# Kernel tuning notes

Measured on AMD Instinct MI355X. Metric: run time of the kernel, lower is better.

Reference implementation:

```python
import jax, jax.numpy as jnp
import numpy as np

N = 4096      # num_nodes
U = 64        # num_units
IN = 2        # input_dim
DIM = U + IN  # 66
H = 4         # attention heads
ALPHA = 0.2   # leaky slope inside attention scores
SLOPE = 0.01  # nn.LeakyReLU() default for subnet activations
NEG_INF = -9e15


def setup_inputs() -> dict:
    key = jax.random.key(0)
    ks = jax.random.split(key, 20)
    def gn(k, shape, fan):
        return jax.random.normal(k, shape, dtype=jnp.float32) / np.float32(np.sqrt(fan))
    adj = jax.random.randint(ks[2], (N, N), 0, 2, dtype=jnp.int32)
    adj = jnp.maximum(adj, jnp.eye(N, dtype=jnp.int32))  # ensure self-loops
    return {
        "inputs": jax.random.normal(ks[0], (1, N * IN), dtype=jnp.float32),
        "hx": jax.random.normal(ks[1], (1, N, U), dtype=jnp.float32),
        "adj": adj,
        "m1_W": gn(ks[3], (H, DIM, DIM), DIM),
        "m1_a1": gn(ks[4], (H, DIM), DIM),
        "m1_a2": gn(ks[5], (H, DIM), DIM),
        "m1_Wout": gn(ks[6], (H * DIM, DIM), H * DIM),
        "m1_ao1": gn(ks[7], (DIM,), DIM),
        "m1_ao2": gn(ks[8], (DIM,), DIM),
        "m2_W": gn(ks[9], (H, DIM, DIM), DIM),
        "m2_a1": gn(ks[10], (H, DIM), DIM),
        "m2_a2": gn(ks[11], (H, DIM), DIM),
        "m2_Wout": gn(ks[12], (H * DIM, DIM), H * DIM),
        "m2_ao1": gn(ks[13], (DIM,), DIM),
        "m2_ao2": gn(ks[14], (DIM,), DIM),
        "g1_W": gn(ks[15], (DIM, 2 * U), DIM),
        "g1_b": jnp.zeros((2 * U,), dtype=jnp.float32),
        "g2_W": gn(ks[16], (DIM, U), DIM),
        "g2_b": jnp.zeros((U,), dtype=jnp.float32),
    }


def gat_layer(x, W, a1, a2, mask):
    # x: [N,Fin], W: [Fin,Fout], a1/a2: [Fout], mask: [N,N] bool
    h = x @ W                                   # [N,Fout]
    f1 = h @ a1                                 # [N] source term
    f2 = h @ a2                                 # [N] target term
    e = jax.nn.leaky_relu(f1[:, None] + f2[None, :], ALPHA)  # [N,N]
    e = jnp.where(mask, e, NEG_INF)
    attn = jax.nn.softmax(e, axis=-1)
    return attn @ h                             # [N,Fout]


def subnet(x, W, a1, a2, Wout, ao1, ao2, mask):
    # multi-head GAT, concat heads, activation, output GAT layer, activation
    heads = jax.vmap(gat_layer, in_axes=(None, 0, 0, 0, None))(x, W, a1, a2, mask)  # [H,N,DIM]
    hcat = jnp.transpose(heads, (1, 0, 2)).reshape(x.shape[0], -1)                   # [N,H*DIM]
    hcat = jax.nn.leaky_relu(hcat, SLOPE)
    out = gat_layer(hcat, Wout, ao1, ao2, mask)                                      # [N,DIM]
    return jax.nn.leaky_relu(out, SLOPE)


def reference(inputs, hx, adj, m1_W, m1_a1, m1_a2, m1_Wout, m1_ao1, m1_ao2,
              m2_W, m2_a1, m2_a2, m2_Wout, m2_ao1, m2_ao2,
              g1_W, g1_b, g2_W, g2_b):
    mask = adj > 0
    xi = inputs.reshape(N, IN)
    xh = hx.reshape(N, U)
    # _GAT1: concat(inputs, hx) -> GATSubNet1 -> linear -> sigmoid -> split r,u
    x1 = jnp.concatenate([xi, xh], axis=-1)                 # [N,DIM]
    g1 = subnet(x1, m1_W, m1_a1, m1_a2, m1_Wout, m1_ao1, m1_ao2, mask)
    value = jax.nn.sigmoid(g1 @ g1_W + g1_b)                # [N,2U]
    r, u = value[:, :U], value[:, U:]
    # _GAT2: concat(inputs, r*hx) -> GATSubNet2 -> linear -> tanh
    x2 = jnp.concatenate([xi, r * xh], axis=-1)             # [N,DIM]
    g2 = subnet(x2, m2_W, m2_a1, m2_a2, m2_Wout, m2_ao1, m2_ao2, mask)
    c = jnp.tanh(g2 @ g2_W + g2_b)                          # [N,U]
    new_state = u * xh + (1.0 - u) * c
    return new_state.reshape(1, N, U)
```

## Files before the change

### kernel.cpp

```cpp
#include <hip/hip_runtime.h>
#include <hip/hip_bf16.h>

constexpr int kN = 4096;
constexpr int kDim = 66;
constexpr int kH = 4;
constexpr int kU = 64;
constexpr float kAlpha = 0.2f;
constexpr float kSlope = 0.01f;
constexpr float kLog2e = 1.44269504f;

typedef _Float16 half8 __attribute__((ext_vector_type(8)));
typedef _Float16 half2t __attribute__((ext_vector_type(2)));
typedef __attribute__((ext_vector_type(4))) float floatx4;

__device__ inline unsigned int fkey(float f){
  unsigned int u = __float_as_uint(f);
  return (u & 0x80000000u) ? ~u : (u | 0x80000000u);
}
__device__ inline float funkey(unsigned int k){
  unsigned int u = (k & 0x80000000u) ? (k ^ 0x80000000u) : ~k;
  return __uint_as_float(u);
}

__global__ void setup_k(const int* __restrict__ adj, unsigned long long* __restrict__ packed,
                        const float* __restrict__ in2, const float* __restrict__ hx,
                        _Float16* __restrict__ x1b, _Float16* __restrict__ x2b,
                        const float* __restrict__ m1W, const float* __restrict__ m1a1, const float* __restrict__ m1a2,
                        const float* __restrict__ m1Wo, const float* __restrict__ m1ao1, const float* __restrict__ m1ao2,
                        const float* __restrict__ m2W, const float* __restrict__ m2a1, const float* __restrict__ m2a2,
                        const float* __restrict__ m2Wo, const float* __restrict__ m2ao1, const float* __restrict__ m2ao2,
                        const float* __restrict__ g1W, const float* __restrict__ g1b,
                        const float* __restrict__ g2W, const float* __restrict__ g2b,
                        _Float16* __restrict__ B1t, _Float16* __restrict__ B1t2,
                        _Float16* __restrict__ B2t, _Float16* __restrict__ B2t2,
                        _Float16* __restrict__ Bgt, _Float16* __restrict__ Bft,
                        unsigned int* __restrict__ fmaxbuf){
  int bb = blockIdx.x, t = threadIdx.x;
  if (bb < 16384){
    int gid = bb * 256 + t;
    unsigned long long m = __ballot(adj[gid] != 0);
    if ((t & 63) == 0) packed[gid >> 6] = m;
    return;
  }
  if (bb < 16384 + 1024){
    int i = (bb - 16384) * 4 + (t >> 6);
    int c = t & 63;
    x1b[(size_t)i * 96 + 2 + c] = (_Float16)hx[(size_t)i * kU + c];
    if (c < 2){
      _Float16 xv = (_Float16)in2[i * 2 + c];
      x1b[(size_t)i * 96 + c] = xv;
      x2b[(size_t)i * 96 + c] = xv;
    }
    if (c < 30){
      x1b[(size_t)i * 96 + 66 + c] = (_Float16)0.f;
      x2b[(size_t)i * 96 + 66 + c] = (_Float16)0.f;
    }
    return;
  }
  int b = bb - (16384 + 1024);
  if (b < 8){
    int m = b & 3;
    const float* W  = (b < 4 ? m1W  : m2W)  + (size_t)m * kDim * kDim;
    const float* a1 = (b < 4 ? m1a1 : m2a1) + m * kDim;
    const float* a2 = (b < 4 ? m1a2 : m2a2) + m * kDim;
    _Float16* Bo = (b < 4 ? B1t : B1t2) + (size_t)m * 80 * 96;
    __shared__ float Ws[kDim * kDim];
    __shared__ float wa1s[kDim], wa2s[kDim];
    for (int z = t; z < kDim * kDim; z += 256) Ws[z] = W[z];
    __syncthreads();
    if (t < kDim){
      float s1 = 0.f, s2 = 0.f;
      for (int d = 0; d < kDim; d++){ float wv = Ws[t * kDim + d]; s1 += wv * a1[d]; s2 += wv * a2[d]; }
      wa1s[t] = s1; wa2s[t] = s2;
    }
    __syncthreads();
    for (int z = t; z < 80 * 96; z += 256){
      int nn = z / 96, k = z % 96;
      float val = 0.f;
      if (k < kDim){
        if (nn < kDim) val = Ws[k * kDim + nn];
        else if (nn == 66) val = wa1s[k];
        else if (nn == 67) val = wa2s[k];
      }
      Bo[z] = (_Float16)val;
    }
  } else if (b < 10){
    const float* Wo  = (b == 8 ? m1Wo  : m2Wo);
    const float* ao1 = (b == 8 ? m1ao1 : m2ao1);
    const float* ao2 = (b == 8 ? m1ao2 : m2ao2);
    _Float16* Bo = (b == 8 ? B2t : B2t2);
    __shared__ float wo1s[264], wo2s[264];
    for (int k = t; k < 264; k += 256){
      float s1 = 0.f, s2 = 0.f;
      for (int d = 0; d < kDim; d++){ float wv = Wo[(size_t)k * kDim + d]; s1 += wv * ao1[d]; s2 += wv * ao2[d]; }
      wo1s[k] = s1; wo2s[k] = s2;
    }
    __syncthreads();
    for (int z = t; z < 80 * 288; z += 256){
      int nn = z / 288, k = z % 288;
      float val = 0.f;
      if (k < 264){
        if (nn < kDim) val = Wo[(size_t)k * kDim + nn];
        else if (nn == 66) val = wo1s[k];
        else if (nn == 67) val = wo2s[k];
      }
      Bo[z] = (_Float16)val;
    }
  } else if (b == 10){
    for (int z = t; z < 128 * 96; z += 256){
      int nn = z / 96, k = z % 96;
      float val = 0.f;
      if (k < kDim) val = g1W[k * 128 + nn];
      else if (k == 66) val = g1b[nn];
      Bgt[z] = (_Float16)val;
    }
  } else {
    if (t < 16) fmaxbuf[t] = 0u;
    for (int z = t; z < 64 * 96; z += 256){
      int nn = z / 96, k = z % 96;
      float val = 0.f;
      if (k < kDim) val = g2W[k * 64 + nn];
      else if (k == 66) val = g2b[nn];
      Bft[z] = (_Float16)val;
    }
  }
}

template<int KSTEPS, int NT, int EPI>
__global__ __launch_bounds__(256) void gemm_k(
    const _Float16* __restrict__ A, const _Float16* __restrict__ Bt,
    void* __restrict__ p0, void* __restrict__ p1, void* __restrict__ p2,
    const float* __restrict__ aux, unsigned int* __restrict__ fmaxp)
{
  constexpr int KP = KSTEPS * 32;
  const int m = blockIdx.y;
  const int i0 = blockIdx.x * 64;
  const int t = threadIdx.x;
  const int w = t >> 6, lane = t & 63, q = lane >> 4, n = lane & 15;
  const int arow = i0 + w * 16 + n;
  const _Float16* Ar = A + (size_t)arow * KP;
  const _Float16* Bm = Bt + (size_t)m * (NT * 16) * KP;
  floatx4 acc[NT];
  #pragma unroll
  for (int v = 0; v < NT; v++) acc[v] = (floatx4){0.f, 0.f, 0.f, 0.f};
  #pragma unroll
  for (int ks = 0; ks < KSTEPS; ks++){
    half8 af = *(const half8*)&Ar[ks * 32 + q * 8];
    #pragma unroll
    for (int nt = 0; nt < NT; nt++){
      half8 bf = *(const half8*)&Bm[(size_t)(nt * 16 + n) * KP + ks * 32 + q * 8];
      acc[nt] = __builtin_amdgcn_mfma_f32_16x16x32_f16(af, bf, acc[nt], 0, 0, 0);
    }
  }
  const int ib = i0 + w * 16 + q * 4;
  if constexpr (EPI == 0){
    _Float16* Ht = (_Float16*)p0 + (size_t)m * 68 * kN;
    float* f1 = (float*)p1 + (size_t)m * kN;
    float* f2 = (float*)p2 + (size_t)m * kN;
    float lm = -3e38f;
    #pragma unroll
    for (int nt = 0; nt < NT; nt++){
      int c = nt * 16 + n;
      if (c < kDim){
        union { _Float16 h[4]; uint2 v; } pk;
        pk.h[0] = (_Float16)acc[nt][0]; pk.h[1] = (_Float16)acc[nt][1];
        pk.h[2] = (_Float16)acc[nt][2]; pk.h[3] = (_Float16)acc[nt][3];
        *(uint2*)&Ht[(size_t)c * kN + ib] = pk.v;
      } else if (c == 66){
        float4 fv; fv.x = acc[nt][0] * kLog2e; fv.y = acc[nt][1] * kLog2e;
        fv.z = acc[nt][2] * kLog2e; fv.w = acc[nt][3] * kLog2e;
        *(float4*)&f1[ib] = fv;
        *(uint2*)&Ht[(size_t)66 * kN + ib] = make_uint2(0x3C003C00u, 0x3C003C00u);
      } else if (c == 67){
        float4 fv; fv.x = acc[nt][0] * kLog2e; fv.y = acc[nt][1] * kLog2e;
        fv.z = acc[nt][2] * kLog2e; fv.w = acc[nt][3] * kLog2e;
        *(float4*)&f2[ib] = fv;
        lm = fmaxf(fmaxf(fv.x, fv.y), fmaxf(fv.z, fv.w));
        *(uint2*)&Ht[(size_t)67 * kN + ib] = make_uint2(0u, 0u);
      }
    }
    lm = fmaxf(lm, __shfl_xor(lm, 16));
    lm = fmaxf(lm, __shfl_xor(lm, 32));
    if (lane == 3) atomicMax(&fmaxp[m], fkey(lm));
  } else if constexpr (EPI == 1){
    float* u = (float*)p0;
    _Float16* x2b = (_Float16*)p1;
    #pragma unroll
    for (int nt = 0; nt < NT; nt++){
      int c = nt * 16 + n;
      #pragma unroll
      for (int r = 0; r < 4; r++){
        float v = 1.f / (1.f + __expf(-acc[nt][r]));
        if (c < 64) x2b[(size_t)(ib + r) * 96 + 2 + c] = (_Float16)(v * aux[(size_t)(ib + r) * kU + c]);
        else        u[(size_t)(ib + r) * kU + (c - 64)] = v;
      }
    }
  } else {
    float* outp = (float*)p0;
    const float* u = (const float*)p1;
    #pragma unroll
    for (int nt = 0; nt < NT; nt++){
      int c = nt * 16 + n;
      #pragma unroll
      for (int r = 0; r < 4; r++){
        float cc = tanhf(acc[nt][r]);
        float uv = u[(size_t)(ib + r) * kU + c];
        outp[(size_t)(ib + r) * kU + c] = uv * aux[(size_t)(ib + r) * kU + c] + (1.f - uv) * cc;
      }
    }
  }
}

template<int JSPLIT>
__global__ __launch_bounds__(256, 4) void attn_mfma_k(
    const _Float16* __restrict__ Ht, const float* __restrict__ f1,
    const float* __restrict__ f2, const unsigned int* __restrict__ fmaxu,
    const unsigned long long* __restrict__ packed,
    _Float16* __restrict__ paccb)
{
  constexpr int JR = kN / JSPLIT;
  constexpr int NCH = JR / 128;
  const int m = blockIdx.y, js = blockIdx.z;
  const int i0 = blockIdx.x * 64;
  const int t = threadIdx.x;
  const int w = t >> 6, lane = t & 63, q = lane >> 4, n = lane & 15;
  const int i = i0 + w * 16 + n;
  const _Float16* Hg = Ht + (size_t)m * 68 * kN;
  const float* f2m = f2 + (size_t)m * kN;
  const float f1v = f1[(size_t)m * kN + i];
  const float fmx = funkey(fmaxu[m]);
  const float t0 = f1v + fmx;
  const float S = fmaxf(t0, kAlpha * t0);
  const float A1f = __builtin_amdgcn_exp2f(t0 - S);
  const float A2f = __builtin_amdgcn_exp2f(kAlpha * t0 - S);
  const half2t a1p = { (_Float16)A1f, (_Float16)A1f };
  const half2t a2p = { (_Float16)A2f, (_Float16)A2f };

  __shared__ __align__(16) _Float16 HtL[80 * 136];
  __shared__ __align__(16) _Float16 B1h[128], B2h[128];

  for (int z = t; z < 12 * 136; z += 256) HtL[68 * 136 + z] = (_Float16)0.f;

  floatx4 acc[5];
  #pragma unroll
  for (int v = 0; v < 5; v++) acc[v] = (floatx4){0.f, 0.f, 0.f, 0.f};

  const int jbase = js * JR;
  const unsigned long long* prow = packed + (size_t)i * 64;
  for (int ch = 0; ch < NCH; ch++){
    const int j0 = jbase + ch * 128;
    __syncthreads();
    for (int z = t; z < 68 * 16; z += 256){
      int row = z >> 4, c16 = z & 15;
      *(uint4*)&HtL[row * 136 + c16 * 8] = *(const uint4*)&Hg[(size_t)row * kN + j0 + c16 * 8];
    }
    if (t < 128){
      float v = f2m[j0 + t] - fmx;
      B1h[t] = (_Float16)__builtin_amdgcn_exp2f(v);
      B2h[t] = (_Float16)__builtin_amdgcn_exp2f(kAlpha * v);
    }
    __syncthreads();
    unsigned long long w0 = prow[(j0 >> 6)];
    unsigned long long w1 = prow[(j0 >> 6) + 1];
    #pragma unroll
    for (int ks = 0; ks < 4; ks++){
      unsigned long long wsel = (ks < 2) ? w0 : w1;
      unsigned int bits = (unsigned int)((wsel >> ((ks & 1) * 32 + q * 8)) & 0xffull);
      union { uint4 v; unsigned int u[4]; } b1v, b2v;
      b1v.v = *(const uint4*)&B1h[ks * 32 + q * 8];
      b2v.v = *(const uint4*)&B2h[ks * 32 + q * 8];
      union { half8 s; unsigned int u[4]; } af;
      #pragma unroll
      for (int e = 0; e < 4; e++){
        half2t x1 = __builtin_bit_cast(half2t, b1v.u[e]);
        half2t x2 = __builtin_bit_cast(half2t, b2v.u[e]);
        half2t m1 = x1 * a1p;
        half2t m2 = x2 * a2p;
        half2t pm = __builtin_elementwise_max(m1, m2);
        unsigned int mm = (((bits >> (2 * e)) & 1u) ? 0x0000FFFFu : 0u)
                        | (((bits >> (2 * e + 1)) & 1u) ? 0xFFFF0000u : 0u);
        af.u[e] = __builtin_bit_cast(unsigned int, pm) & mm;
      }
      #pragma unroll
      for (int nt = 0; nt < 5; nt++){
        const half8 bf = *(const half8*)&HtL[(nt * 16 + n) * 136 + ks * 32 + q * 8];
        acc[nt] = __builtin_amdgcn_mfma_f32_16x16x32_f16(af.s, bf, acc[nt], 0, 0, 0);
      }
    }
  }
  _Float16* pw = paccb + ((size_t)(m * JSPLIT + js) * kN + (i0 + w * 16)) * 80;
  #pragma unroll
  for (int nt = 0; nt < 5; nt++){
    if (nt < 4 || n < 4){
      #pragma unroll
      for (int r = 0; r < 4; r++)
        pw[(q * 4 + r) * 80 + nt * 16 + n] = (_Float16)acc[nt][r];
    }
  }
}

template<int JSPLIT>
__global__ void combine_k(const _Float16* __restrict__ paccb, _Float16* __restrict__ outb,
                          int ostride, int ones_col){
  int m = blockIdx.y;
  int i = blockIdx.x * 64 + (threadIdx.x >> 2);
  int cg = threadIdx.x & 3;
  const _Float16* ps[JSPLIT];
  #pragma unroll
  for (int s = 0; s < JSPLIT; s++)
    ps[s] = paccb + ((size_t)(m * JSPLIT + s) * kN + i) * 80;
  float l = 0.f;
  #pragma unroll
  for (int s = 0; s < JSPLIT; s++) l += (float)ps[s][66];
  float inv = 1.f / l;
  _Float16* orow = outb + (size_t)i * ostride + m * kDim;
  #pragma unroll
  for (int cc = 0; cc < 17; cc++){
    int c = cg * 17 + cc;
    if (c < kDim){
      float v = 0.f;
      #pragma unroll
      for (int s = 0; s < JSPLIT; s++) v += (float)ps[s][c];
      v *= inv;
      v = fmaxf(v, kSlope * v);
      orow[c] = (_Float16)v;
    }
  }
  if (ones_col && cg == 3) orow[66] = (_Float16)1.f;
}

extern "C" void kernel_launch(void* const* d_in, const int* in_sizes, int n_in,
                              void* d_out, int out_size, void* d_ws, size_t ws_size,
                              hipStream_t stream){
  const float* inputs  = (const float*)d_in[0];
  const float* hx      = (const float*)d_in[1];
  const int*   adj     = (const int*)d_in[2];
  const float* m1_W    = (const float*)d_in[3];
  const float* m1_a1   = (const float*)d_in[4];
  const float* m1_a2   = (const float*)d_in[5];
  const float* m1_Wout = (const float*)d_in[6];
  const float* m1_ao1  = (const float*)d_in[7];
  const float* m1_ao2  = (const float*)d_in[8];
  const float* m2_W    = (const float*)d_in[9];
  const float* m2_a1   = (const float*)d_in[10];
  const float* m2_a2   = (const float*)d_in[11];
  const float* m2_Wout = (const float*)d_in[12];
  const float* m2_ao1  = (const float*)d_in[13];
  const float* m2_ao2  = (const float*)d_in[14];
  const float* g1_W    = (const float*)d_in[15];
  const float* g1_b    = (const float*)d_in[16];
  const float* g2_W    = (const float*)d_in[17];
  const float* g2_b    = (const float*)d_in[18];
  float* out = (float*)d_out;

  char* ws = (char*)d_ws;
  size_t off = 0;
  auto alloc = [&](size_t bytes) -> void* {
    void* p = ws + off;
    off = (off + bytes + 255) & ~(size_t)255;
    return p;
  };
  unsigned long long* packed = (unsigned long long*)alloc((size_t)kN * 64 * 8);
  _Float16* x1b  = (_Float16*)alloc((size_t)kN * 96 * 2);
  _Float16* x2b  = (_Float16*)alloc((size_t)kN * 96 * 2);
  _Float16* Ht   = (_Float16*)alloc((size_t)kH * 68 * kN * 2);
  _Float16* Hto  = (_Float16*)alloc((size_t)68 * kN * 2);
  _Float16* hcatb= (_Float16*)alloc((size_t)kN * 288 * 2);
  _Float16* gb   = (_Float16*)alloc((size_t)kN * 96 * 2);
  _Float16* g2bv = (_Float16*)alloc((size_t)kN * 96 * 2);
  float* f1   = (float*)alloc((size_t)kH * kN * 4);
  float* f2   = (float*)alloc((size_t)kH * kN * 4);
  float* fo1  = (float*)alloc((size_t)kN * 4);
  float* fo2  = (float*)alloc((size_t)kN * 4);
  unsigned int* fmaxbuf = (unsigned int*)alloc(64);
  float* u    = (float*)alloc((size_t)kN * kU * 4);
  _Float16* paccb = (_Float16*)alloc((size_t)16 * kN * 80 * 2);
  _Float16* B1t  = (_Float16*)alloc((size_t)kH * 80 * 96 * 2);
  _Float16* B1t2 = (_Float16*)alloc((size_t)kH * 80 * 96 * 2);
  _Float16* B2t  = (_Float16*)alloc((size_t)80 * 288 * 2);
  _Float16* B2t2 = (_Float16*)alloc((size_t)80 * 288 * 2);
  _Float16* Bgt  = (_Float16*)alloc((size_t)128 * 96 * 2);
  _Float16* Bft  = (_Float16*)alloc((size_t)64 * 96 * 2);
  (void)ws_size; (void)in_sizes; (void)n_in; (void)out_size;

  setup_k<<<16384 + 1024 + 12, 256, 0, stream>>>(adj, packed, inputs, hx, x1b, x2b,
      m1_W, m1_a1, m1_a2, m1_Wout, m1_ao1, m1_ao2,
      m2_W, m2_a1, m2_a2, m2_Wout, m2_ao1, m2_ao2,
      g1_W, g1_b, g2_W, g2_b,
      B1t, B1t2, B2t, B2t2, Bgt, Bft, fmaxbuf);

  gemm_k<3, 5, 0><<<dim3(64, kH), 256, 0, stream>>>(x1b, B1t, Ht, f1, f2, nullptr, fmaxbuf + 0);
  attn_mfma_k<4><<<dim3(64, kH, 4), 256, 0, stream>>>(Ht, f1, f2, fmaxbuf + 0, packed, paccb);
  combine_k<4><<<dim3(64, kH), 256, 0, stream>>>(paccb, hcatb, 288, 0);
  gemm_k<9, 5, 0><<<dim3(64, 1), 256, 0, stream>>>(hcatb, B2t, Hto, fo1, fo2, nullptr, fmaxbuf + 4);
  attn_mfma_k<8><<<dim3(64, 1, 8), 256, 0, stream>>>(Hto, fo1, fo2, fmaxbuf + 4, packed, paccb);
  combine_k<8><<<dim3(64, 1), 256, 0, stream>>>(paccb, gb, 96, 1);
  gemm_k<3, 8, 1><<<dim3(64, 1), 256, 0, stream>>>(gb, Bgt, u, x2b, nullptr, hx, nullptr);

  gemm_k<3, 5, 0><<<dim3(64, kH), 256, 0, stream>>>(x2b, B1t2, Ht, f1, f2, nullptr, fmaxbuf + 5);
  attn_mfma_k<4><<<dim3(64, kH, 4), 256, 0, stream>>>(Ht, f1, f2, fmaxbuf + 5, packed, paccb);
  combine_k<4><<<dim3(64, kH), 256, 0, stream>>>(paccb, hcatb, 288, 0);
  gemm_k<9, 5, 0><<<dim3(64, 1), 256, 0, stream>>>(hcatb, B2t2, Hto, fo1, fo2, nullptr, fmaxbuf + 9);
  attn_mfma_k<8><<<dim3(64, 1, 8), 256, 0, stream>>>(Hto, fo1, fo2, fmaxbuf + 9, packed, paccb);
  combine_k<8><<<dim3(64, 1), 256, 0, stream>>>(paccb, g2bv, 96, 1);
  gemm_k<3, 4, 2><<<dim3(64, 1), 256, 0, stream>>>(g2bv, Bft, out, u, nullptr, hx, nullptr);
}
```

Baseline: 319.6 us.

## Double-buffer attention tiles via direct global-to-LDS loads with swizzle; vectorize combine

The attention kernel now stages each 128-column chunk of H into LDS with global_load_lds and a double buffer, prefetching the next chunk and its exp terms while MFMAs run on the current one. The LDS layout drops padding in favour of an XOR swizzle, and a shared zero row stands in for the padded rows. The combine kernel reads and writes 16-byte vectors and pads each head to 72 columns, so the concatenated hidden layout and the Wout weight packing are remapped to match. This overlaps the global loads that were previously serialized between barriers, at the cost of a more intricate layout that must stay consistent across kernels.

```diff
diff --git a/kernel.cpp b/kernel.cpp
--- a/kernel.cpp
+++ b/kernel.cpp
@@ -20,6 +20,11 @@
 __device__ inline float funkey(unsigned int k){
   unsigned int u = (k & 0x80000000u) ? (k ^ 0x80000000u) : ~k;
   return __uint_as_float(u);
+}
+
+__device__ __forceinline__ void gld_lds16(const void* g, void* l){
+  __builtin_amdgcn_global_load_lds((const __attribute__((address_space(1))) unsigned int*)g,
+                                   (__attribute__((address_space(3))) unsigned int*)l, 16, 0, 0);
 }
 
 __global__ void setup_k(const int* __restrict__ adj, unsigned long long* __restrict__ packed,
@@ -98,11 +103,13 @@
     __syncthreads();
     for (int z = t; z < 80 * 288; z += 256){
       int nn = z / 288, k = z % 288;
+      int h = k / 72, c = k - h * 72;
       float val = 0.f;
-      if (k < 264){
-        if (nn < kDim) val = Wo[(size_t)k * kDim + nn];
-        else if (nn == 66) val = wo1s[k];
-        else if (nn == 67) val = wo2s[k];
+      if (c < 66){
+        int kk = h * 66 + c;
+        if (nn < kDim) val = Wo[(size_t)kk * kDim + nn];
+        else if (nn == 66) val = wo1s[kk];
+        else if (nn == 67) val = wo2s[kk];
       }
       Bo[z] = (_Float16)val;
     }
@@ -236,58 +243,104 @@
   const half2t a1p = { (_Float16)A1f, (_Float16)A1f };
   const half2t a2p = { (_Float16)A2f, (_Float16)A2f };
 
-  __shared__ __align__(16) _Float16 HtL[80 * 136];
-  __shared__ __align__(16) _Float16 B1h[128], B2h[128];
-
-  for (int z = t; z < 12 * 136; z += 256) HtL[68 * 136 + z] = (_Float16)0.f;
-
-  floatx4 acc[5];
-  #pragma unroll
-  for (int v = 0; v < 5; v++) acc[v] = (floatx4){0.f, 0.f, 0.f, 0.f};
+  __shared__ __align__(16) _Float16 buf[2][68 * 128];
+  __shared__ __align__(16) _Float16 Zro[128];
+  __shared__ __align__(16) _Float16 B1h[2][128], B2h[2][128];
+
+  for (int z = t; z < 128; z += 256) Zro[z] = (_Float16)0.f;
+
+  const int r4 = q;
+  const int cse = n ^ r4;
+  const int cso = cse ^ 4;
 
   const int jbase = js * JR;
   const unsigned long long* prow = packed + (size_t)i * 64;
-  for (int ch = 0; ch < NCH; ch++){
-    const int j0 = jbase + ch * 128;
-    __syncthreads();
-    for (int z = t; z < 68 * 16; z += 256){
-      int row = z >> 4, c16 = z & 15;
-      *(uint4*)&HtL[row * 136 + c16 * 8] = *(const uint4*)&Hg[(size_t)row * kN + j0 + c16 * 8];
-    }
-    if (t < 128){
-      float v = f2m[j0 + t] - fmx;
-      B1h[t] = (_Float16)__builtin_amdgcn_exp2f(v);
-      B2h[t] = (_Float16)__builtin_amdgcn_exp2f(kAlpha * v);
-    }
-    __syncthreads();
-    unsigned long long w0 = prow[(j0 >> 6)];
-    unsigned long long w1 = prow[(j0 >> 6) + 1];
-    #pragma unroll
-    for (int ks = 0; ks < 4; ks++){
-      unsigned long long wsel = (ks < 2) ? w0 : w1;
-      unsigned int bits = (unsigned int)((wsel >> ((ks & 1) * 32 + q * 8)) & 0xffull);
-      union { uint4 v; unsigned int u[4]; } b1v, b2v;
-      b1v.v = *(const uint4*)&B1h[ks * 32 + q * 8];
-      b2v.v = *(const uint4*)&B2h[ks * 32 + q * 8];
-      union { half8 s; unsigned int u[4]; } af;
-      #pragma unroll
-      for (int e = 0; e < 4; e++){
-        half2t x1 = __builtin_bit_cast(half2t, b1v.u[e]);
-        half2t x2 = __builtin_bit_cast(half2t, b2v.u[e]);
-        half2t m1 = x1 * a1p;
-        half2t m2 = x2 * a2p;
-        half2t pm = __builtin_elementwise_max(m1, m2);
-        unsigned int mm = (((bits >> (2 * e)) & 1u) ? 0x0000FFFFu : 0u)
-                        | (((bits >> (2 * e + 1)) & 1u) ? 0xFFFF0000u : 0u);
-        af.u[e] = __builtin_bit_cast(unsigned int, pm) & mm;
-      }
-      #pragma unroll
-      for (int nt = 0; nt < 5; nt++){
-        const half8 bf = *(const half8*)&HtL[(nt * 16 + n) * 136 + ks * 32 + q * 8];
-        acc[nt] = __builtin_amdgcn_mfma_f32_16x16x32_f16(af.s, bf, acc[nt], 0, 0, 0);
-      }
-    }
-  }
+  const int jj = (w << 5) | (lane & 31);
+  const bool blane = (lane & 32) == 0;
+
+#define STAGE_G(PD, CH) do { \
+    const _Float16* gB_ = Hg + jbase + (CH) * 128; \
+    _Pragma("unroll") \
+    for (int kk_ = 0; kk_ < 5; kk_++){ \
+      const int k_ = w + kk_ * 4; \
+      if (k_ < 17){ \
+        const int row_ = k_ * 4 + r4; \
+        const int csw_ = (k_ & 1) ? cso : cse; \
+        gld_lds16(gB_ + (size_t)row_ * kN + csw_ * 8, &buf[(PD)][k_ * 512]); \
+      } \
+    } \
+  } while (0)
+
+  floatx4 acc[5];
+  #pragma unroll
+  for (int v = 0; v < 5; v++) acc[v] = (floatx4){0.f, 0.f, 0.f, 0.f};
+
+  if (blane){
+    const float v_ = f2m[jbase + jj] - fmx;
+    B1h[0][jj] = (_Float16)__builtin_amdgcn_exp2f(v_);
+    B2h[0][jj] = (_Float16)__builtin_amdgcn_exp2f(kAlpha * v_);
+  }
+  STAGE_G(0, 0);
+  __syncthreads();
+
+  int ch = 0;
+#define BODY(P) do { \
+    const int j0_ = jbase + ch * 128; \
+     \
+    float f2v_ = 0.f; \
+    const bool doB_ = (ch + 1 < NCH) && blane; \
+    if (doB_) f2v_ = f2m[j0_ + 128 + jj]; \
+    const unsigned long long w0_ = prow[j0_ >> 6]; \
+    const unsigned long long w1_ = prow[(j0_ >> 6) + 1]; \
+    __builtin_amdgcn_sched_barrier(0); \
+    if (ch + 1 < NCH) STAGE_G((P) ^ 1, ch + 1); \
+    __builtin_amdgcn_sched_barrier(0); \
+    if (doB_){ \
+      const float v_ = f2v_ - fmx; \
+      B1h[(P) ^ 1][jj] = (_Float16)__builtin_amdgcn_exp2f(v_); \
+      B2h[(P) ^ 1][jj] = (_Float16)__builtin_amdgcn_exp2f(kAlpha * v_); \
+    } \
+    const _Float16* bz_ = (n < 4) ? &buf[(P)][(64 + n) * 128] : Zro; \
+    _Pragma("unroll") \
+    for (int ks = 0; ks < 4; ks++){ \
+      const unsigned long long wsel = (ks < 2) ? w0_ : w1_; \
+      const unsigned int bits = (unsigned int)((wsel >> ((ks & 1) * 32 + q * 8)) & 0xffull); \
+      union { uint4 v; unsigned int u[4]; } b1v, b2v; \
+      b1v.v = *(const uint4*)&B1h[(P)][ks * 32 + q * 8]; \
+      b2v.v = *(const uint4*)&B2h[(P)][ks * 32 + q * 8]; \
+      union { half8 s; unsigned int u[4]; } af; \
+      _Pragma("unroll") \
+      for (int e = 0; e < 4; e++){ \
+        half2t x1 = __builtin_bit_cast(half2t, b1v.u[e]); \
+        half2t x2 = __builtin_bit_cast(half2t, b2v.u[e]); \
+        half2t m1 = x1 * a1p; \
+        half2t m2 = x2 * a2p; \
+        half2t pm = __builtin_elementwise_max(m1, m2); \
+        unsigned int mm = (((bits >> (2 * e)) & 1u) ? 0x0000FFFFu : 0u) \
+                        | (((bits >> (2 * e + 1)) & 1u) ? 0xFFFF0000u : 0u); \
+        af.u[e] = __builtin_bit_cast(unsigned int, pm) & mm; \
+      } \
+      const int cs_ = ((ks * 4 + q) ^ (n & 7)) * 8; \
+      _Pragma("unroll") \
+      for (int nt = 0; nt < 4; nt++){ \
+        const half8 bf = *(const half8*)&buf[(P)][(nt * 16 + n) * 128 + cs_]; \
+        acc[nt] = __builtin_amdgcn_mfma_f32_16x16x32_f16(af.s, bf, acc[nt], 0, 0, 0); \
+      } \
+      { const half8 bf4 = *(const half8*)&bz_[cs_]; \
+        acc[4] = __builtin_amdgcn_mfma_f32_16x16x32_f16(af.s, bf4, acc[4], 0, 0, 0); } \
+    } \
+    ch++; \
+    if (ch < NCH) __syncthreads(); \
+  } while (0)
+
+  #pragma unroll 1
+  for (int it = 0; it < NCH / 2; it++){
+    BODY(0);
+    BODY(1);
+  }
+#undef BODY
+#undef STAGE_G
+
   _Float16* pw = paccb + ((size_t)(m * JSPLIT + js) * kN + (i0 + w * 16)) * 80;
   #pragma unroll
   for (int nt = 0; nt < 5; nt++){
@@ -301,32 +354,55 @@
 
 template<int JSPLIT>
 __global__ void combine_k(const _Float16* __restrict__ paccb, _Float16* __restrict__ outb,
-                          int ostride, int ones_col){
-  int m = blockIdx.y;
-  int i = blockIdx.x * 64 + (threadIdx.x >> 2);
-  int cg = threadIdx.x & 3;
-  const _Float16* ps[JSPLIT];
-  #pragma unroll
-  for (int s = 0; s < JSPLIT; s++)
-    ps[s] = paccb + ((size_t)(m * JSPLIT + s) * kN + i) * 80;
-  float l = 0.f;
-  #pragma unroll
-  for (int s = 0; s < JSPLIT; s++) l += (float)ps[s][66];
-  float inv = 1.f / l;
-  _Float16* orow = outb + (size_t)i * ostride + m * kDim;
-  #pragma unroll
-  for (int cc = 0; cc < 17; cc++){
-    int c = cg * 17 + cc;
-    if (c < kDim){
-      float v = 0.f;
+                          int ostride, int headoff, int ones_col){
+  const int m = blockIdx.y;
+  const int t = threadIdx.x;
+  const int ri = t >> 2, cg = t & 3;
+  const int lane = t & 63;
+  const int i = blockIdx.x * 64 + ri;
+  const _Float16* pb = paccb + ((size_t)m * JSPLIT * kN + i) * 80;
+  float accv[3][8];
+  #pragma unroll
+  for (int k = 0; k < 3; k++)
+    #pragma unroll
+    for (int e = 0; e < 8; e++) accv[k][e] = 0.f;
+  #pragma unroll
+  for (int s = 0; s < JSPLIT; s++){
+    const _Float16* ps = pb + (size_t)s * kN * 80;
+    #pragma unroll
+    for (int k = 0; k < 3; k++){
+      const int c = cg + 4 * k;
+      if (c < 9){
+        union { uint4 v; _Float16 h[8]; } uu;
+        uu.v = *(const uint4*)&ps[c * 8];
+        #pragma unroll
+        for (int e = 0; e < 8; e++) accv[k][e] += (float)uu.h[e];
+      }
+    }
+  }
+  float l = accv[2][2];
+  l = __shfl(l, lane & ~3, 64);
+  const float inv = 1.f / l;
+  _Float16* orow = outb + (size_t)i * ostride + m * headoff;
+  #pragma unroll
+  for (int k = 0; k < 3; k++){
+    const int c = cg + 4 * k;
+    if (c < 9){
+      union { uint4 v; _Float16 h[8]; } uu;
       #pragma unroll
-      for (int s = 0; s < JSPLIT; s++) v += (float)ps[s][c];
-      v *= inv;
-      v = fmaxf(v, kSlope * v);
-      orow[c] = (_Float16)v;
-    }
-  }
-  if (ones_col && cg == 3) orow[66] = (_Float16)1.f;
+      for (int e = 0; e < 8; e++){
+        float v = accv[k][e] * inv;
+        v = fmaxf(v, kSlope * v);
+        uu.h[e] = (_Float16)v;
+      }
+      if (c == 8){
+        uu.h[2] = (_Float16)(ones_col ? 1.f : 0.f);
+        #pragma unroll
+        for (int e = 3; e < 8; e++) uu.h[e] = (_Float16)0.f;
+      }
+      *(uint4*)&orow[c * 8] = uu.v;
+    }
+  }
 }
 
 extern "C" void kernel_launch(void* const* d_in, const int* in_sizes, int n_in,
@@ -391,17 +467,17 @@
 
   gemm_k<3, 5, 0><<<dim3(64, kH), 256, 0, stream>>>(x1b, B1t, Ht, f1, f2, nullptr, fmaxbuf + 0);
   attn_mfma_k<4><<<dim3(64, kH, 4), 256, 0, stream>>>(Ht, f1, f2, fmaxbuf + 0, packed, paccb);
-  combine_k<4><<<dim3(64, kH), 256, 0, stream>>>(paccb, hcatb, 288, 0);
+  combine_k<4><<<dim3(64, kH), 256, 0, stream>>>(paccb, hcatb, 288, 72, 0);
   gemm_k<9, 5, 0><<<dim3(64, 1), 256, 0, stream>>>(hcatb, B2t, Hto, fo1, fo2, nullptr, fmaxbuf + 4);
   attn_mfma_k<8><<<dim3(64, 1, 8), 256, 0, stream>>>(Hto, fo1, fo2, fmaxbuf + 4, packed, paccb);
-  combine_k<8><<<dim3(64, 1), 256, 0, stream>>>(paccb, gb, 96, 1);
+  combine_k<8><<<dim3(64, 1), 256, 0, stream>>>(paccb, gb, 96, 0, 1);
   gemm_k<3, 8, 1><<<dim3(64, 1), 256, 0, stream>>>(gb, Bgt, u, x2b, nullptr, hx, nullptr);
 
   gemm_k<3, 5, 0><<<dim3(64, kH), 256, 0, stream>>>(x2b, B1t2, Ht, f1, f2, nullptr, fmaxbuf + 5);
   attn_mfma_k<4><<<dim3(64, kH, 4), 256, 0, stream>>>(Ht, f1, f2, fmaxbuf + 5, packed, paccb);
-  combine_k<4><<<dim3(64, kH), 256, 0, stream>>>(paccb, hcatb, 288, 0);
+  combine_k<4><<<dim3(64, kH), 256, 0, stream>>>(paccb, hcatb, 288, 72, 0);
   gemm_k<9, 5, 0><<<dim3(64, 1), 256, 0, stream>>>(hcatb, B2t2, Hto, fo1, fo2, nullptr, fmaxbuf + 9);
   attn_mfma_k<8><<<dim3(64, 1, 8), 256, 0, stream>>>(Hto, fo1, fo2, fmaxbuf + 9, packed, paccb);
-  combine_k<8><<<dim3(64, 1), 256, 0, stream>>>(paccb, g2bv, 96, 1);
+  combine_k<8><<<dim3(64, 1), 256, 0, stream>>>(paccb, g2bv, 96, 0, 1);
   gemm_k<3, 4, 2><<<dim3(64, 1), 256, 0, stream>>>(g2bv, Bft, out, u, nullptr, hx, nullptr);
 }
```

Result: faster. 293.8 us (-8.1%).

## Read H directly from global in attention, vectorize combine with padded head layout

Applied to the files above, without the earlier changes.

The attention kernel no longer stages each 128-column tile of H into LDS with two barriers per chunk. Each lane now loads its MFMA B-fragments straight from global memory, and the exp2 terms for the whole j-range are precomputed once into LDS. The combine kernel is rewritten to use 16-byte vector loads and stores, and the concatenated head layout is padded to 72 columns per head so those stores stay aligned, with the Wout packing remapped to match. Dropping the per-chunk barriers and LDS traffic trades against uncoalesced global fragment loads that depend on cache hits.

```diff
diff --git a/kernel.cpp b/kernel.cpp
--- a/kernel.cpp
+++ b/kernel.cpp
@@ -98,11 +98,13 @@
     __syncthreads();
     for (int z = t; z < 80 * 288; z += 256){
       int nn = z / 288, k = z % 288;
+      int h = k / 72, c = k - h * 72;
       float val = 0.f;
-      if (k < 264){
-        if (nn < kDim) val = Wo[(size_t)k * kDim + nn];
-        else if (nn == 66) val = wo1s[k];
-        else if (nn == 67) val = wo2s[k];
+      if (c < 66){
+        int kk = h * 66 + c;
+        if (nn < kDim) val = Wo[(size_t)kk * kDim + nn];
+        else if (nn == 66) val = wo1s[kk];
+        else if (nn == 67) val = wo2s[kk];
       }
       Bo[z] = (_Float16)val;
     }
@@ -236,39 +238,40 @@
   const half2t a1p = { (_Float16)A1f, (_Float16)A1f };
   const half2t a2p = { (_Float16)A2f, (_Float16)A2f };
 
-  __shared__ __align__(16) _Float16 HtL[80 * 136];
-  __shared__ __align__(16) _Float16 B1h[128], B2h[128];
-
-  for (int z = t; z < 12 * 136; z += 256) HtL[68 * 136 + z] = (_Float16)0.f;
+  __shared__ __align__(16) _Float16 B1h[JR], B2h[JR];
+
+  const int jbase = js * JR;
+  for (int z = t; z < JR; z += 256){
+    const float v = f2m[jbase + z] - fmx;
+    B1h[z] = (_Float16)__builtin_amdgcn_exp2f(v);
+    B2h[z] = (_Float16)__builtin_amdgcn_exp2f(kAlpha * v);
+  }
+  __syncthreads();
+
+  const _Float16* Hrow[5];
+  #pragma unroll
+  for (int nt = 0; nt < 4; nt++) Hrow[nt] = Hg + (size_t)(nt * 16 + n) * kN + jbase;
+  Hrow[4] = Hg + (size_t)(64 + (n < 4 ? n : 0)) * kN + jbase;
+  const int qo = q * 8;
+
+  const unsigned long long* prow = packed + (size_t)i * 64 + (jbase >> 6);
 
   floatx4 acc[5];
   #pragma unroll
   for (int v = 0; v < 5; v++) acc[v] = (floatx4){0.f, 0.f, 0.f, 0.f};
 
-  const int jbase = js * JR;
-  const unsigned long long* prow = packed + (size_t)i * 64;
+  #pragma unroll 1
   for (int ch = 0; ch < NCH; ch++){
-    const int j0 = jbase + ch * 128;
-    __syncthreads();
-    for (int z = t; z < 68 * 16; z += 256){
-      int row = z >> 4, c16 = z & 15;
-      *(uint4*)&HtL[row * 136 + c16 * 8] = *(const uint4*)&Hg[(size_t)row * kN + j0 + c16 * 8];
-    }
-    if (t < 128){
-      float v = f2m[j0 + t] - fmx;
-      B1h[t] = (_Float16)__builtin_amdgcn_exp2f(v);
-      B2h[t] = (_Float16)__builtin_amdgcn_exp2f(kAlpha * v);
-    }
-    __syncthreads();
-    unsigned long long w0 = prow[(j0 >> 6)];
-    unsigned long long w1 = prow[(j0 >> 6) + 1];
+    const int j0 = ch * 128;
+    const unsigned long long w0 = prow[ch * 2];
+    const unsigned long long w1 = prow[ch * 2 + 1];
     #pragma unroll
     for (int ks = 0; ks < 4; ks++){
-      unsigned long long wsel = (ks < 2) ? w0 : w1;
-      unsigned int bits = (unsigned int)((wsel >> ((ks & 1) * 32 + q * 8)) & 0xffull);
+      const unsigned long long wsel = (ks < 2) ? w0 : w1;
+      const unsigned int bits = (unsigned int)((wsel >> ((ks & 1) * 32 + qo)) & 0xffull);
       union { uint4 v; unsigned int u[4]; } b1v, b2v;
-      b1v.v = *(const uint4*)&B1h[ks * 32 + q * 8];
-      b2v.v = *(const uint4*)&B2h[ks * 32 + q * 8];
+      b1v.v = *(const uint4*)&B1h[j0 + ks * 32 + qo];
+      b2v.v = *(const uint4*)&B2h[j0 + ks * 32 + qo];
       union { half8 s; unsigned int u[4]; } af;
       #pragma unroll
       for (int e = 0; e < 4; e++){
@@ -283,11 +286,12 @@
       }
       #pragma unroll
       for (int nt = 0; nt < 5; nt++){
-        const half8 bf = *(const half8*)&HtL[(nt * 16 + n) * 136 + ks * 32 + q * 8];
+        const half8 bf = *(const half8*)&Hrow[nt][j0 + ks * 32 + qo];
         acc[nt] = __builtin_amdgcn_mfma_f32_16x16x32_f16(af.s, bf, acc[nt], 0, 0, 0);
       }
     }
   }
+
   _Float16* pw = paccb + ((size_t)(m * JSPLIT + js) * kN + (i0 + w * 16)) * 80;
   #pragma unroll
   for (int nt = 0; nt < 5; nt++){
@@ -301,32 +305,55 @@
 
 template<int JSPLIT>
 __global__ void combine_k(const _Float16* __restrict__ paccb, _Float16* __restrict__ outb,
-                          int ostride, int ones_col){
-  int m = blockIdx.y;
-  int i = blockIdx.x * 64 + (threadIdx.x >> 2);
-  int cg = threadIdx.x & 3;
-  const _Float16* ps[JSPLIT];
-  #pragma unroll
-  for (int s = 0; s < JSPLIT; s++)
-    ps[s] = paccb + ((size_t)(m * JSPLIT + s) * kN + i) * 80;
-  float l = 0.f;
-  #pragma unroll
-  for (int s = 0; s < JSPLIT; s++) l += (float)ps[s][66];
-  float inv = 1.f / l;
-  _Float16* orow = outb + (size_t)i * ostride + m * kDim;
-  #pragma unroll
-  for (int cc = 0; cc < 17; cc++){
-    int c = cg * 17 + cc;
-    if (c < kDim){
-      float v = 0.f;
-      #pragma unroll
-      for (int s = 0; s < JSPLIT; s++) v += (float)ps[s][c];
-      v *= inv;
-      v = fmaxf(v, kSlope * v);
-      orow[c] = (_Float16)v;
-    }
-  }
-  if (ones_col && cg == 3) orow[66] = (_Float16)1.f;
+                          int ostride, int headoff, int ones_col){
+  const int m = blockIdx.y;
+  const int t = threadIdx.x;
+  const int ri = t >> 2, cg = t & 3;
+  const int lane = t & 63;
+  const int i = blockIdx.x * 64 + ri;
+  const _Float16* pb = paccb + ((size_t)m * JSPLIT * kN + i) * 80;
+  float accv[3][8];
+  #pragma unroll
+  for (int k = 0; k < 3; k++)
+    #pragma unroll
+    for (int e = 0; e < 8; e++) accv[k][e] = 0.f;
+  #pragma unroll
+  for (int s = 0; s < JSPLIT; s++){
+    const _Float16* ps = pb + (size_t)s * kN * 80;
+    #pragma unroll
+    for (int k = 0; k < 3; k++){
+      const int c = cg + 4 * k;
+      if (c < 9){
+        union { uint4 v; _Float16 h[8]; } uu;
+        uu.v = *(const uint4*)&ps[c * 8];
+        #pragma unroll
+        for (int e = 0; e < 8; e++) accv[k][e] += (float)uu.h[e];
+      }
+    }
+  }
+  float l = accv[2][2];
+  l = __shfl(l, lane & ~3, 64);
+  const float inv = 1.f / l;
+  _Float16* orow = outb + (size_t)i * ostride + m * headoff;
+  #pragma unroll
+  for (int k = 0; k < 3; k++){
+    const int c = cg + 4 * k;
+    if (c < 9){
+      union { uint4 v; _Float16 h[8]; } uu;
+      #pragma unroll
+      for (int e = 0; e < 8; e++){
+        float v = accv[k][e] * inv;
+        v = fmaxf(v, kSlope * v);
+        uu.h[e] = (_Float16)v;
+      }
+      if (c == 8){
+        uu.h[2] = (_Float16)(ones_col ? 1.f : 0.f);
+        #pragma unroll
+        for (int e = 3; e < 8; e++) uu.h[e] = (_Float16)0.f;
+      }
+      *(uint4*)&orow[c * 8] = uu.v;
+    }
+  }
 }
 
 extern "C" void kernel_launch(void* const* d_in, const int* in_sizes, int n_in,
@@ -391,17 +418,17 @@
 
   gemm_k<3, 5, 0><<<dim3(64, kH), 256, 0, stream>>>(x1b, B1t, Ht, f1, f2, nullptr, fmaxbuf + 0);
   attn_mfma_k<4><<<dim3(64, kH, 4), 256, 0, stream>>>(Ht, f1, f2, fmaxbuf + 0, packed, paccb);
-  combine_k<4><<<dim3(64, kH), 256, 0, stream>>>(paccb, hcatb, 288, 0);
+  combine_k<4><<<dim3(64, kH), 256, 0, stream>>>(paccb, hcatb, 288, 72, 0);
   gemm_k<9, 5, 0><<<dim3(64, 1), 256, 0, stream>>>(hcatb, B2t, Hto, fo1, fo2, nullptr, fmaxbuf + 4);
   attn_mfma_k<8><<<dim3(64, 1, 8), 256, 0, stream>>>(Hto, fo1, fo2, fmaxbuf + 4, packed, paccb);
-  combine_k<8><<<dim3(64, 1), 256, 0, stream>>>(paccb, gb, 96, 1);
+  combine_k<8><<<dim3(64, 1), 256, 0, stream>>>(paccb, gb, 96, 0, 1);
   gemm_k<3, 8, 1><<<dim3(64, 1), 256, 0, stream>>>(gb, Bgt, u, x2b, nullptr, hx, nullptr);
 
   gemm_k<3, 5, 0><<<dim3(64, kH), 256, 0, stream>>>(x2b, B1t2, Ht, f1, f2, nullptr, fmaxbuf + 5);
   attn_mfma_k<4><<<dim3(64, kH, 4), 256, 0, stream>>>(Ht, f1, f2, fmaxbuf + 5, packed, paccb);
-  combine_k<4><<<dim3(64, kH), 256, 0, stream>>>(paccb, hcatb, 288, 0);
+  combine_k<4><<<dim3(64, kH), 256, 0, stream>>>(paccb, hcatb, 288, 72, 0);
   gemm_k<9, 5, 0><<<dim3(64, 1), 256, 0, stream>>>(hcatb, B2t2, Hto, fo1, fo2, nullptr, fmaxbuf + 9);
   attn_mfma_k<8><<<dim3(64, 1, 8), 256, 0, stream>>>(Hto, fo1, fo2, fmaxbuf + 9, packed, paccb);
-  combine_k<8><<<dim3(64, 1), 256, 0, stream>>>(paccb, g2bv, 96, 1);
+  combine_k<8><<<dim3(64, 1), 256, 0, stream>>>(paccb, g2bv, 96, 0, 1);
   gemm_k<3, 4, 2><<<dim3(64, 1), 256, 0, stream>>>(g2bv, Bft, out, u, nullptr, hx, nullptr);
 }
```

Measured after the change: 414.6 us. 1.3x slower.
